# Optimization experiments

Measured on AMD Instinct MI355X. Metric: run time of the kernel, lower is better.

## Reference

```python
import jax, jax.numpy as jnp
import numpy as np

RATIO = 0.5
BN_EPS = 1e-5
L2_EPS = 1e-8


def setup_inputs() -> dict:
    key = jax.random.key(0)
    ks = jax.random.split(key, 8)
    B, L, D, E = 64, 577, 512, 1024
    H = E // 2  # MLP hidden = embed_dim // 2 = 512
    base_features = jax.random.normal(ks[0], (B, L, D), dtype=jnp.float32)
    atten = jax.random.uniform(ks[1], (B, L, L), dtype=jnp.float32)
    s_fc = 1.0 / np.sqrt(D)
    s_h = 1.0 / np.sqrt(H)
    return {
        "base_features": base_features,
        "atten": atten,
        "fc_w": jax.random.uniform(ks[2], (E, D), jnp.float32, -s_fc, s_fc),
        "fc_b": jax.random.uniform(ks[3], (E,), jnp.float32, -s_fc, s_fc),
        "mlp_w0": jax.random.uniform(ks[4], (H, D), jnp.float32, -s_fc, s_fc),
        "mlp_b0": jax.random.uniform(ks[5], (H,), jnp.float32, -s_fc, s_fc),
        "bn0_gamma": jnp.ones((H,), jnp.float32),
        "bn0_beta": jnp.zeros((H,), jnp.float32),
        "mlp_w1": jax.random.uniform(ks[6], (E, H), jnp.float32, -s_h, s_h),
        "mlp_b1": jax.random.uniform(ks[7], (E,), jnp.float32, -s_h, s_h),
    }


def _forward(base_features, atten, fc_w, fc_b, mlp_w0, mlp_b0,
             bn0_gamma, bn0_beta, mlp_w1, mlp_b1):
    B, L, D = base_features.shape
    k = int((L - 1) * RATIO)  # static: derived from shape

    # atten[:, :, 0] = -1; rank tokens by CLS-row attention atten[:, 0]
    scores = atten[:, 0].at[:, 0].set(-1.0)           # [B, L]
    idx = jax.lax.top_k(scores, k)[1]                 # [B, k]

    # gather selected tokens: [B, k, D]
    feats = jnp.take_along_axis(base_features, idx[:, :, None], axis=1)

    # l2norm over last dim (norm = sqrt(sum(x^2)) + eps, then divide)
    norm = jnp.sqrt(jnp.sum(feats * feats, axis=-1, keepdims=True)) + L2_EPS
    feats = feats / norm

    # MLP (num_layers=2): Linear -> BN(training-mode batch stats) -> ReLU -> Linear
    x = feats.reshape(B * k, D)
    h = x @ mlp_w0.T + mlp_b0                         # [B*k, H]
    mu = jnp.mean(h, axis=0)
    var = jnp.mean((h - mu) ** 2, axis=0)             # biased var, as torch BN
    h = jax.nn.relu(bn0_gamma * (h - mu) * jax.lax.rsqrt(var + BN_EPS) + bn0_beta)
    x_att = (h @ mlp_w1.T + mlp_b1).reshape(B, k, -1)  # [B, k, E]

    local = jnp.einsum('bkd,ed->bke', feats, fc_w) + fc_b + x_att

    # maxk_pool1d_var with k=1 and full lengths == max over sequence dim
    return jnp.max(local, axis=1).astype(jnp.float32)  # [B, E]


def reference(base_features, atten, fc_w, fc_b, mlp_w0, mlp_b0,
              bn0_gamma, bn0_beta, mlp_w1, mlp_b1):
    return _forward(base_features, atten, fc_w, fc_b, mlp_w0, mlp_b0,
                    bn0_gamma, bn0_beta, mlp_w1, mlp_b1)
```

## Files before the change

kernel.cpp:

```cpp
#include <hip/hip_runtime.h>
#include <math.h>

#define B_   64
#define L_   577
#define D_   512
#define E_   1024
#define H_   512
#define K_   288
#define N_   (B_ * K_)
#define KBIG 1024
#define MTILES (N_ / 128)

typedef __attribute__((ext_vector_type(8))) __bf16 bf16x8;
typedef __attribute__((ext_vector_type(4))) float f32x4;
typedef __attribute__((ext_vector_type(4))) unsigned short ushort4v;
typedef __attribute__((ext_vector_type(8))) unsigned short ushort8v;

#define OFF_WBIG    0
#define OFF_W0B     2097152
#define OFF_BIASBIG 2621440
#define OFF_SCSH    2625536
#define OFF_IDX     2629632
#define OFF_PSUM    2703360
#define OFF_PSQ     2998272
#define OFF_OUTENC  3293184
#define OFF_ABIG    3555328

static __device__ __forceinline__ unsigned short f2bf(float f) {
  unsigned int u = __builtin_bit_cast(unsigned int, f);
  u = (u + 0x7fffu + ((u >> 16) & 1u)) >> 16;
  return (unsigned short)u;
}
static __device__ __forceinline__ float bf2f(unsigned short s) {
  unsigned int u = ((unsigned int)s) << 16;
  return __builtin_bit_cast(float, u);
}

static __device__ __forceinline__ unsigned int encf(float f) {
  unsigned int u = __builtin_bit_cast(unsigned int, f);
  return (u & 0x80000000u) ? ~u : (u | 0x80000000u);
}
static __device__ __forceinline__ float decf(unsigned int e) {
  unsigned int u = (e & 0x80000000u) ? (e ^ 0x80000000u) : ~e;
  return __builtin_bit_cast(float, u);
}

#define GLOAD_LDS16(g, l)                                          \
  __builtin_amdgcn_global_load_lds(                                \
      (const __attribute__((address_space(1))) void*)(g),          \
      (__attribute__((address_space(3))) void*)(l), 16, 0, 0)

__global__ __launch_bounds__(256) void prep_kernel(
    const float* __restrict__ fc_w, const float* __restrict__ fc_b,
    const float* __restrict__ w0,   const float* __restrict__ w1,
    const float* __restrict__ b1,
    unsigned short* __restrict__ wbig, unsigned short* __restrict__ w0b,
    float* __restrict__ biasbig, unsigned int* __restrict__ outenc) {
  int gid = blockIdx.x * 256 + threadIdx.x;
  if (gid < 65536) outenc[gid] = 0u;
  if (gid < 262144) {
    int e  = gid >> 8;
    int c4 = gid & 255;
    float4 v;
    if (c4 < 128) v = ((const float4*)(fc_w + e * D_))[c4];
    else          v = ((const float4*)(w1   + e * H_))[c4 - 128];
    ushort4v o = { f2bf(v.x), f2bf(v.y), f2bf(v.z), f2bf(v.w) };
    ((ushort4v*)wbig)[gid] = o;
    if (gid < E_) biasbig[gid] = fc_b[gid] + b1[gid];
  } else {
    int idx = gid - 262144;
    float4 v = ((const float4*)w0)[idx];
    ushort4v o = { f2bf(v.x), f2bf(v.y), f2bf(v.z), f2bf(v.w) };
    ((ushort4v*)w0b)[idx] = o;
  }
}

__global__ __launch_bounds__(256) void topk_kernel(
    const float* __restrict__ atten, int* __restrict__ idx) {
  __shared__ float s[L_];
  int b = blockIdx.x;
  const float* row = atten + (size_t)b * L_ * L_;
  for (int i = threadIdx.x; i < L_; i += 256) s[i] = (i == 0) ? -1.0f : row[i];
  __syncthreads();
  for (int i = threadIdx.x; i < L_; i += 256) {
    float si = s[i];
    int rank = 0;
    for (int j = 0; j < L_; ++j) {
      float sj = s[j];
      rank += (sj > si) || (sj == si && j < i);
    }
    if (rank < K_) idx[b * K_ + rank] = i;
  }
}

__global__ __launch_bounds__(128) void gather_norm_kernel(
    const float* __restrict__ base, const int* __restrict__ idx,
    unsigned short* __restrict__ abig) {
  int r = blockIdx.x;
  int b = r / K_;
  int tok = idx[r];
  const float* src = base + ((size_t)b * L_ + tok) * D_;
  float4 v = ((const float4*)src)[threadIdx.x];
  float ss = v.x * v.x + v.y * v.y + v.z * v.z + v.w * v.w;
  #pragma unroll
  for (int o = 32; o > 0; o >>= 1) ss += __shfl_down(ss, o, 64);
  __shared__ float wsum[2];
  if ((threadIdx.x & 63) == 0) wsum[threadIdx.x >> 6] = ss;
  __syncthreads();
  float total = wsum[0] + wsum[1];
  float inv = 1.0f / (sqrtf(total) + 1e-8f);
  ushort4v o4 = { f2bf(v.x * inv), f2bf(v.y * inv), f2bf(v.z * inv), f2bf(v.w * inv) };
  ((ushort4v*)(abig + (size_t)r * KBIG))[threadIdx.x] = o4;
}

template <int MODE>
__global__ __launch_bounds__(256) void gemm_mfma_kernel(
    const unsigned short* __restrict__ A, int lda,
    const unsigned short* __restrict__ W, int ldw,
    const float* __restrict__ bias,
    unsigned short* __restrict__ Cbf, int ldc, int K,
    float* __restrict__ psum, float* __restrict__ psq,
    unsigned int* __restrict__ outenc) {
  __shared__ unsigned short As[128 * 64];
  __shared__ unsigned short Bs[128 * 64];
  __shared__ float s_sum[4][64];
  __shared__ float s_sq[4][64];
  const int tid  = threadIdx.x;
  const int wave = tid >> 6;
  const int lane = tid & 63;
  const int m0 = blockIdx.x * 128;
  const int n0 = blockIdx.y * 128;

  const int srow = wave * 8 + (lane >> 3);
  const int g8   = ((lane & 7) ^ ((lane >> 3) & 7)) * 8;
  const int ldst = (wave * 64 + lane) * 8;

  const int quad = lane >> 4;
  const int l15  = lane & 15;
  const int wm = (wave & 1) * 64;
  const int wn = (wave >> 1) * 64;
  const int slot0 = quad ^ (l15 & 7);

  f32x4 acc[4][4];
  #pragma unroll
  for (int i = 0; i < 4; ++i)
    #pragma unroll
    for (int j = 0; j < 4; ++j)
      acc[i][j] = (f32x4)(0.0f);

  for (int k0 = 0; k0 < K; k0 += 64) {
    #pragma unroll
    for (int q = 0; q < 4; ++q) {
      GLOAD_LDS16(A + (size_t)(m0 + q * 32 + srow) * lda + k0 + g8,
                  &As[q * 2048 + ldst]);
      GLOAD_LDS16(W + (size_t)(n0 + q * 32 + srow) * ldw + k0 + g8,
                  &Bs[q * 2048 + ldst]);
    }
    __syncthreads();
    #pragma unroll
    for (int kk = 0; kk < 2; ++kk) {
      const int slot = slot0 ^ (kk * 4);
      bf16x8 af[4], bfr[4];
      #pragma unroll
      for (int i = 0; i < 4; ++i)
        af[i] = *(const bf16x8*)&As[(wm + 16 * i + l15) * 64 + slot * 8];
      #pragma unroll
      for (int j = 0; j < 4; ++j)
        bfr[j] = *(const bf16x8*)&Bs[(wn + 16 * j + l15) * 64 + slot * 8];
      #pragma unroll
      for (int i = 0; i < 4; ++i)
        #pragma unroll
        for (int j = 0; j < 4; ++j)
          acc[i][j] = __builtin_amdgcn_mfma_f32_16x16x32_bf16(af[i], bfr[j], acc[i][j], 0, 0, 0);
    }
    __syncthreads();
  }

  if (MODE == 0) {
    #pragma unroll
    for (int j = 0; j < 4; ++j) {
      int col = n0 + wn + 16 * j + l15;
      float bb = bias[col];
      float sm = 0.f, sq = 0.f;
      #pragma unroll
      for (int i = 0; i < 4; ++i) {
        int row_base = m0 + wm + 16 * i + quad * 4;
        #pragma unroll
        for (int r = 0; r < 4; ++r) {
          float v = acc[i][j][r] + bb;
          Cbf[(size_t)(row_base + r) * ldc + col] = f2bf(v);
          sm += v; sq += v * v;
        }
      }
      sm += __shfl_xor(sm, 16, 64); sm += __shfl_xor(sm, 32, 64);
      sq += __shfl_xor(sq, 16, 64); sq += __shfl_xor(sq, 32, 64);
      if (quad == 0) { s_sum[wave][j * 16 + l15] = sm; s_sq[wave][j * 16 + l15] = sq; }
    }
    __syncthreads();
    if (tid < 128) {
      int half = tid >> 6;
      int c = tid & 63;
      float sm = s_sum[half * 2][c] + s_sum[half * 2 + 1][c];
      float sq = s_sq[half * 2][c] + s_sq[half * 2 + 1][c];
      int col = n0 + half * 64 + c;
      psum[blockIdx.x * H_ + col] = sm;
      psq [blockIdx.x * H_ + col] = sq;
    }
  } else {
    #pragma unroll
    for (int j = 0; j < 4; ++j) {
      int col = n0 + wn + 16 * j + l15;
      float bb = bias[col];
      float m[4];
      #pragma unroll
      for (int i = 0; i < 4; ++i) {
        float v = fmaxf(fmaxf(acc[i][j][0], acc[i][j][1]),
                        fmaxf(acc[i][j][2], acc[i][j][3]));
        m[i] = v + bb;
      }
      #pragma unroll
      for (int i = 0; i < 4; ++i) {
        m[i] = fmaxf(m[i], __shfl_xor(m[i], 16, 64));
        m[i] = fmaxf(m[i], __shfl_xor(m[i], 32, 64));
      }
      if (quad == 0) {
        int base = m0 + wm;
        int b0i = (base) / K_;
        float cur = m[0]; int cb = b0i;
        #pragma unroll
        for (int i = 1; i < 4; ++i) {
          int bi = (base + 16 * i) / K_;
          if (bi == cb) cur = fmaxf(cur, m[i]);
          else { atomicMax(&outenc[cb * E_ + col], encf(cur)); cur = m[i]; cb = bi; }
        }
        atomicMax(&outenc[cb * E_ + col], encf(cur));
      }
    }
  }
}

__global__ __launch_bounds__(256) void bn_stats2_kernel(
    const float* __restrict__ psum, const float* __restrict__ psq,
    const float* __restrict__ gamma, const float* __restrict__ beta,
    float* __restrict__ scsh) {
  __shared__ float ls[8][32], lq[8][32];
  int c32 = threadIdx.x & 31;
  int slice = threadIdx.x >> 5;
  int c = blockIdx.x * 32 + c32;
  float S = 0.f, Q = 0.f;
  for (int i = 0; i < 18; ++i) {
    int mx = slice * 18 + i;
    S += psum[mx * H_ + c];
    Q += psq [mx * H_ + c];
  }
  ls[slice][c32] = S; lq[slice][c32] = Q;
  __syncthreads();
  if (slice == 0) {
    float St = 0.f, Qt = 0.f;
    #pragma unroll
    for (int s = 0; s < 8; ++s) { St += ls[s][c32]; Qt += lq[s][c32]; }
    const float invN = 1.0f / (float)N_;
    float mu = St * invN;
    float var = Qt * invN - mu * mu;
    float sc = rsqrtf(var + 1e-5f) * gamma[c];
    scsh[c] = sc;
    scsh[512 + c] = beta[c] - mu * sc;
  }
}

__global__ __launch_bounds__(256) void bn_apply_kernel(
    unsigned short* __restrict__ abig, const float* __restrict__ scsh) {
  int gid = blockIdx.x * 256 + threadIdx.x;
  int r = gid >> 6;
  int c8 = gid & 63;
  int c = c8 * 8;
  ushort8v* p = (ushort8v*)(abig + (size_t)r * KBIG + H_) + c8;
  ushort8v v = *p;
  float4 sca = *(const float4*)&scsh[c];
  float4 scb = *(const float4*)&scsh[c + 4];
  float4 sha = *(const float4*)&scsh[512 + c];
  float4 shb = *(const float4*)&scsh[512 + c + 4];
  float sc[8] = {sca.x, sca.y, sca.z, sca.w, scb.x, scb.y, scb.z, scb.w};
  float sh[8] = {sha.x, sha.y, sha.z, sha.w, shb.x, shb.y, shb.z, shb.w};
  ushort8v o;
  #pragma unroll
  for (int j = 0; j < 8; ++j) {
    float x = bf2f(v[j]);
    o[j] = f2bf(fmaxf(x * sc[j] + sh[j], 0.0f));
  }
  *p = o;
}

__global__ __launch_bounds__(256) void decode_kernel(
    const unsigned int* __restrict__ outenc, float* __restrict__ out) {
  int gid = blockIdx.x * 256 + threadIdx.x;
  out[gid] = decf(outenc[gid]);
}

extern "C" void kernel_launch(void* const* d_in, const int* in_sizes, int n_in,
                              void* d_out, int out_size, void* d_ws, size_t ws_size,
                              hipStream_t stream) {
  const float* base  = (const float*)d_in[0];
  const float* atten = (const float*)d_in[1];
  const float* fc_w  = (const float*)d_in[2];
  const float* fc_b  = (const float*)d_in[3];
  const float* w0    = (const float*)d_in[4];
  const float* b0    = (const float*)d_in[5];
  const float* gamma = (const float*)d_in[6];
  const float* beta  = (const float*)d_in[7];
  const float* w1    = (const float*)d_in[8];
  const float* b1    = (const float*)d_in[9];
  float* out = (float*)d_out;

  char* ws = (char*)d_ws;
  unsigned short* wbig    = (unsigned short*)(ws + OFF_WBIG);
  unsigned short* w0b     = (unsigned short*)(ws + OFF_W0B);
  float*          biasbig = (float*)(ws + OFF_BIASBIG);
  float*          scsh    = (float*)(ws + OFF_SCSH);
  int*            idx     = (int*)  (ws + OFF_IDX);
  float*          psum    = (float*)(ws + OFF_PSUM);
  float*          psq     = (float*)(ws + OFF_PSQ);
  unsigned int*   outenc  = (unsigned int*)(ws + OFF_OUTENC);
  unsigned short* abig    = (unsigned short*)(ws + OFF_ABIG);

  prep_kernel<<<1280, 256, 0, stream>>>(fc_w, fc_b, w0, w1, b1, wbig, w0b,
                                        biasbig, outenc);
  topk_kernel<<<B_, 256, 0, stream>>>(atten, idx);
  gather_norm_kernel<<<N_, 128, 0, stream>>>(base, idx, abig);
  {
    dim3 grid(MTILES, H_ / 128);
    gemm_mfma_kernel<0><<<grid, 256, 0, stream>>>(abig, KBIG, w0b, D_, b0,
                                                  abig + H_, KBIG, D_,
                                                  psum, psq, nullptr);
  }
  bn_stats2_kernel<<<16, 256, 0, stream>>>(psum, psq, gamma, beta, scsh);
  bn_apply_kernel<<<(N_ * 64) / 256, 256, 0, stream>>>(abig, scsh);
  {
    dim3 grid(MTILES, E_ / 128);
    gemm_mfma_kernel<1><<<grid, 256, 0, stream>>>(abig, KBIG, wbig, KBIG, biasbig,
                                                  nullptr, 0, KBIG, nullptr, nullptr,
                                                  outenc);
  }
  decode_kernel<<<(B_ * E_) / 256, 256, 0, stream>>>(outenc, out);
}
```

Baseline: 294.4 us.

## Fuse BN-apply into second GEMM loads, merge prep/topk, drop decode

Folds the BatchNorm scale/shift and ReLU into the A-tile load of the second GEMM for the hidden half of K, replacing async LDS loads there with register loads plus conversion. The top-k blocks are merged into the weight-prep kernel as extra blocks, and the output max now uses a float CAS loop written straight to the output, which removes the decode kernel. This cuts three launches and one full read/write pass over the hidden activations. In exchange the fused path gives up async global-to-LDS loads for half the K loop, and CAS loops may contend.

```diff
diff --git a/kernel.cpp b/kernel.cpp
--- a/kernel.cpp
+++ b/kernel.cpp
@@ -23,7 +23,6 @@
 #define OFF_IDX     2629632
 #define OFF_PSUM    2703360
 #define OFF_PSQ     2998272
-#define OFF_OUTENC  3293184
 #define OFF_ABIG    3555328
 
 static __device__ __forceinline__ unsigned short f2bf(float f) {
@@ -36,13 +35,16 @@
   return __builtin_bit_cast(float, u);
 }
 
-static __device__ __forceinline__ unsigned int encf(float f) {
-  unsigned int u = __builtin_bit_cast(unsigned int, f);
-  return (u & 0x80000000u) ? ~u : (u | 0x80000000u);
-}
-static __device__ __forceinline__ float decf(unsigned int e) {
-  unsigned int u = (e & 0x80000000u) ? (e ^ 0x80000000u) : ~e;
-  return __builtin_bit_cast(float, u);
+static __device__ __forceinline__ void atomicMaxF(float* addr, float val) {
+  unsigned int* ua = (unsigned int*)addr;
+  unsigned int vu = __builtin_bit_cast(unsigned int, val);
+  unsigned int cur = __builtin_bit_cast(unsigned int, -INFINITY);
+  while (true) {
+    unsigned int prev = atomicCAS(ua, cur, vu);
+    if (prev == cur) break;
+    if (__builtin_bit_cast(float, prev) >= val) break;
+    cur = prev;
+  }
 }
 
 #define GLOAD_LDS16(g, l)                                          \
@@ -50,46 +52,46 @@
       (const __attribute__((address_space(1))) void*)(g),          \
       (__attribute__((address_space(3))) void*)(l), 16, 0, 0)
 
-__global__ __launch_bounds__(256) void prep_kernel(
+__global__ __launch_bounds__(256) void prep_topk_kernel(
     const float* __restrict__ fc_w, const float* __restrict__ fc_b,
     const float* __restrict__ w0,   const float* __restrict__ w1,
-    const float* __restrict__ b1,
+    const float* __restrict__ b1,   const float* __restrict__ atten,
     unsigned short* __restrict__ wbig, unsigned short* __restrict__ w0b,
-    float* __restrict__ biasbig, unsigned int* __restrict__ outenc) {
-  int gid = blockIdx.x * 256 + threadIdx.x;
-  if (gid < 65536) outenc[gid] = 0u;
-  if (gid < 262144) {
-    int e  = gid >> 8;
-    int c4 = gid & 255;
-    float4 v;
-    if (c4 < 128) v = ((const float4*)(fc_w + e * D_))[c4];
-    else          v = ((const float4*)(w1   + e * H_))[c4 - 128];
-    ushort4v o = { f2bf(v.x), f2bf(v.y), f2bf(v.z), f2bf(v.w) };
-    ((ushort4v*)wbig)[gid] = o;
-    if (gid < E_) biasbig[gid] = fc_b[gid] + b1[gid];
+    float* __restrict__ biasbig, float* __restrict__ out,
+    int* __restrict__ idx) {
+  __shared__ float s[L_];
+  if (blockIdx.x < 1280) {
+    int gid = blockIdx.x * 256 + threadIdx.x;
+    if (gid < 65536) out[gid] = -INFINITY;
+    if (gid < 262144) {
+      int e  = gid >> 8;
+      int c4 = gid & 255;
+      float4 v;
+      if (c4 < 128) v = ((const float4*)(fc_w + e * D_))[c4];
+      else          v = ((const float4*)(w1   + e * H_))[c4 - 128];
+      ushort4v o = { f2bf(v.x), f2bf(v.y), f2bf(v.z), f2bf(v.w) };
+      ((ushort4v*)wbig)[gid] = o;
+      if (gid < E_) biasbig[gid] = fc_b[gid] + b1[gid];
+    } else {
+      int i2 = gid - 262144;
+      float4 v = ((const float4*)w0)[i2];
+      ushort4v o = { f2bf(v.x), f2bf(v.y), f2bf(v.z), f2bf(v.w) };
+      ((ushort4v*)w0b)[i2] = o;
+    }
   } else {
-    int idx = gid - 262144;
-    float4 v = ((const float4*)w0)[idx];
-    ushort4v o = { f2bf(v.x), f2bf(v.y), f2bf(v.z), f2bf(v.w) };
-    ((ushort4v*)w0b)[idx] = o;
-  }
-}
-
-__global__ __launch_bounds__(256) void topk_kernel(
-    const float* __restrict__ atten, int* __restrict__ idx) {
-  __shared__ float s[L_];
-  int b = blockIdx.x;
-  const float* row = atten + (size_t)b * L_ * L_;
-  for (int i = threadIdx.x; i < L_; i += 256) s[i] = (i == 0) ? -1.0f : row[i];
-  __syncthreads();
-  for (int i = threadIdx.x; i < L_; i += 256) {
-    float si = s[i];
-    int rank = 0;
-    for (int j = 0; j < L_; ++j) {
-      float sj = s[j];
-      rank += (sj > si) || (sj == si && j < i);
-    }
-    if (rank < K_) idx[b * K_ + rank] = i;
+    int b = blockIdx.x - 1280;
+    const float* row = atten + (size_t)b * L_ * L_;
+    for (int i = threadIdx.x; i < L_; i += 256) s[i] = (i == 0) ? -1.0f : row[i];
+    __syncthreads();
+    for (int i = threadIdx.x; i < L_; i += 256) {
+      float si = s[i];
+      int rank = 0;
+      for (int j = 0; j < L_; ++j) {
+        float sj = s[j];
+        rank += (sj > si) || (sj == si && j < i);
+      }
+      if (rank < K_) idx[b * K_ + rank] = i;
+    }
   }
 }
 
@@ -120,7 +122,7 @@
     const float* __restrict__ bias,
     unsigned short* __restrict__ Cbf, int ldc, int K,
     float* __restrict__ psum, float* __restrict__ psq,
-    unsigned int* __restrict__ outenc) {
+    const float* __restrict__ scsh, float* __restrict__ outf) {
   __shared__ unsigned short As[128 * 64];
   __shared__ unsigned short Bs[128 * 64];
   __shared__ float s_sum[4][64];
@@ -149,12 +151,36 @@
       acc[i][j] = (f32x4)(0.0f);
 
   for (int k0 = 0; k0 < K; k0 += 64) {
-    #pragma unroll
-    for (int q = 0; q < 4; ++q) {
-      GLOAD_LDS16(A + (size_t)(m0 + q * 32 + srow) * lda + k0 + g8,
-                  &As[q * 2048 + ldst]);
-      GLOAD_LDS16(W + (size_t)(n0 + q * 32 + srow) * ldw + k0 + g8,
-                  &Bs[q * 2048 + ldst]);
+    if (MODE == 0 || k0 < H_) {
+      #pragma unroll
+      for (int q = 0; q < 4; ++q) {
+        GLOAD_LDS16(A + (size_t)(m0 + q * 32 + srow) * lda + k0 + g8,
+                    &As[q * 2048 + ldst]);
+        GLOAD_LDS16(W + (size_t)(n0 + q * 32 + srow) * ldw + k0 + g8,
+                    &Bs[q * 2048 + ldst]);
+      }
+    } else {
+      #pragma unroll
+      for (int q = 0; q < 4; ++q)
+        GLOAD_LDS16(W + (size_t)(n0 + q * 32 + srow) * ldw + k0 + g8,
+                    &Bs[q * 2048 + ldst]);
+      const int c0 = k0 - H_ + g8;
+      float4 sa = *(const float4*)&scsh[c0];
+      float4 sb = *(const float4*)&scsh[c0 + 4];
+      float4 ha = *(const float4*)&scsh[512 + c0];
+      float4 hb = *(const float4*)&scsh[512 + c0 + 4];
+      float sc[8] = {sa.x, sa.y, sa.z, sa.w, sb.x, sb.y, sb.z, sb.w};
+      float sh[8] = {ha.x, ha.y, ha.z, ha.w, hb.x, hb.y, hb.z, hb.w};
+      #pragma unroll
+      for (int q = 0; q < 4; ++q) {
+        ushort8v v = *(const ushort8v*)(A + (size_t)(m0 + q * 32 + srow) * lda
+                                        + k0 + g8);
+        ushort8v o;
+        #pragma unroll
+        for (int j = 0; j < 8; ++j)
+          o[j] = f2bf(fmaxf(bf2f(v[j]) * sc[j] + sh[j], 0.0f));
+        *(ushort8v*)&As[q * 2048 + ldst] = o;
+      }
     }
     __syncthreads();
     #pragma unroll
@@ -225,15 +251,15 @@
       }
       if (quad == 0) {
         int base = m0 + wm;
-        int b0i = (base) / K_;
-        float cur = m[0]; int cb = b0i;
+        int cb = base / K_;
+        float cur = m[0];
         #pragma unroll
         for (int i = 1; i < 4; ++i) {
           int bi = (base + 16 * i) / K_;
           if (bi == cb) cur = fmaxf(cur, m[i]);
-          else { atomicMax(&outenc[cb * E_ + col], encf(cur)); cur = m[i]; cb = bi; }
+          else { atomicMaxF(&outf[cb * E_ + col], cur); cur = m[i]; cb = bi; }
         }
-        atomicMax(&outenc[cb * E_ + col], encf(cur));
+        atomicMaxF(&outf[cb * E_ + col], cur);
       }
     }
   }
@@ -266,35 +292,6 @@
     scsh[c] = sc;
     scsh[512 + c] = beta[c] - mu * sc;
   }
-}
-
-__global__ __launch_bounds__(256) void bn_apply_kernel(
-    unsigned short* __restrict__ abig, const float* __restrict__ scsh) {
-  int gid = blockIdx.x * 256 + threadIdx.x;
-  int r = gid >> 6;
-  int c8 = gid & 63;
-  int c = c8 * 8;
-  ushort8v* p = (ushort8v*)(abig + (size_t)r * KBIG + H_) + c8;
-  ushort8v v = *p;
-  float4 sca = *(const float4*)&scsh[c];
-  float4 scb = *(const float4*)&scsh[c + 4];
-  float4 sha = *(const float4*)&scsh[512 + c];
-  float4 shb = *(const float4*)&scsh[512 + c + 4];
-  float sc[8] = {sca.x, sca.y, sca.z, sca.w, scb.x, scb.y, scb.z, scb.w};
-  float sh[8] = {sha.x, sha.y, sha.z, sha.w, shb.x, shb.y, shb.z, shb.w};
-  ushort8v o;
-  #pragma unroll
-  for (int j = 0; j < 8; ++j) {
-    float x = bf2f(v[j]);
-    o[j] = f2bf(fmaxf(x * sc[j] + sh[j], 0.0f));
-  }
-  *p = o;
-}
-
-__global__ __launch_bounds__(256) void decode_kernel(
-    const unsigned int* __restrict__ outenc, float* __restrict__ out) {
-  int gid = blockIdx.x * 256 + threadIdx.x;
-  out[gid] = decf(outenc[gid]);
 }
 
 extern "C" void kernel_launch(void* const* d_in, const int* in_sizes, int n_in,
@@ -320,26 +317,22 @@
   int*            idx     = (int*)  (ws + OFF_IDX);
   float*          psum    = (float*)(ws + OFF_PSUM);
   float*          psq     = (float*)(ws + OFF_PSQ);
-  unsigned int*   outenc  = (unsigned int*)(ws + OFF_OUTENC);
   unsigned short* abig    = (unsigned short*)(ws + OFF_ABIG);
 
-  prep_kernel<<<1280, 256, 0, stream>>>(fc_w, fc_b, w0, w1, b1, wbig, w0b,
-                                        biasbig, outenc);
-  topk_kernel<<<B_, 256, 0, stream>>>(atten, idx);
+  prep_topk_kernel<<<1344, 256, 0, stream>>>(fc_w, fc_b, w0, w1, b1, atten,
+                                             wbig, w0b, biasbig, out, idx);
   gather_norm_kernel<<<N_, 128, 0, stream>>>(base, idx, abig);
   {
     dim3 grid(MTILES, H_ / 128);
     gemm_mfma_kernel<0><<<grid, 256, 0, stream>>>(abig, KBIG, w0b, D_, b0,
                                                   abig + H_, KBIG, D_,
-                                                  psum, psq, nullptr);
+                                                  psum, psq, nullptr, nullptr);
   }
   bn_stats2_kernel<<<16, 256, 0, stream>>>(psum, psq, gamma, beta, scsh);
-  bn_apply_kernel<<<(N_ * 64) / 256, 256, 0, stream>>>(abig, scsh);
   {
     dim3 grid(MTILES, E_ / 128);
     gemm_mfma_kernel<1><<<grid, 256, 0, stream>>>(abig, KBIG, wbig, KBIG, biasbig,
                                                   nullptr, 0, KBIG, nullptr, nullptr,
-                                                  outenc);
-  }
-  decode_kernel<<<(B_ * E_) / 256, 256, 0, stream>>>(outenc, out);
-}
+                                                  scsh, out);
+  }
+}
```

After: 296.8 us. No clear change (+0.8%).

## Merge prep and topk kernels, atomic BN stats, wave-per-row gather

Applied to the files above, without the earlier changes.

Fuses the weight-prep and top-k kernels into a single launch, with the extra blocks handling per-batch top-k ranking. The BN partial sums are now accumulated with global atomicAdd straight from the first GEMM epilogue, which removes the per-tile partial buffers and shrinks the stats kernel to a trivial per-column finalize. The gather/l2norm kernel maps one wave per row and reduces with shuffles only, so it no longer needs a shared-memory barrier. In exchange, atomics add contention on 1024 floats and make the floating-point summation order nondeterministic.

```diff
diff --git a/kernel.cpp b/kernel.cpp
--- a/kernel.cpp
+++ b/kernel.cpp
@@ -22,7 +22,6 @@
 #define OFF_SCSH    2625536
 #define OFF_IDX     2629632
 #define OFF_PSUM    2703360
-#define OFF_PSQ     2998272
 #define OFF_OUTENC  3293184
 #define OFF_ABIG    3555328
 
@@ -50,67 +49,70 @@
       (const __attribute__((address_space(1))) void*)(g),          \
       (__attribute__((address_space(3))) void*)(l), 16, 0, 0)
 
-__global__ __launch_bounds__(256) void prep_kernel(
+__global__ __launch_bounds__(256) void prep_topk_kernel(
     const float* __restrict__ fc_w, const float* __restrict__ fc_b,
     const float* __restrict__ w0,   const float* __restrict__ w1,
-    const float* __restrict__ b1,
+    const float* __restrict__ b1,   const float* __restrict__ atten,
     unsigned short* __restrict__ wbig, unsigned short* __restrict__ w0b,
-    float* __restrict__ biasbig, unsigned int* __restrict__ outenc) {
-  int gid = blockIdx.x * 256 + threadIdx.x;
-  if (gid < 65536) outenc[gid] = 0u;
-  if (gid < 262144) {
-    int e  = gid >> 8;
-    int c4 = gid & 255;
-    float4 v;
-    if (c4 < 128) v = ((const float4*)(fc_w + e * D_))[c4];
-    else          v = ((const float4*)(w1   + e * H_))[c4 - 128];
-    ushort4v o = { f2bf(v.x), f2bf(v.y), f2bf(v.z), f2bf(v.w) };
-    ((ushort4v*)wbig)[gid] = o;
-    if (gid < E_) biasbig[gid] = fc_b[gid] + b1[gid];
+    float* __restrict__ biasbig, unsigned int* __restrict__ outenc,
+    float* __restrict__ psumq, int* __restrict__ idx) {
+  __shared__ float s[L_];
+  if (blockIdx.x < 1280) {
+    int gid = blockIdx.x * 256 + threadIdx.x;
+    if (gid < 65536) outenc[gid] = 0u;
+    if (gid < 1024) psumq[gid] = 0.0f;
+    if (gid < 262144) {
+      int e  = gid >> 8;
+      int c4 = gid & 255;
+      float4 v;
+      if (c4 < 128) v = ((const float4*)(fc_w + e * D_))[c4];
+      else          v = ((const float4*)(w1   + e * H_))[c4 - 128];
+      ushort4v o = { f2bf(v.x), f2bf(v.y), f2bf(v.z), f2bf(v.w) };
+      ((ushort4v*)wbig)[gid] = o;
+      if (gid < E_) biasbig[gid] = fc_b[gid] + b1[gid];
+    } else {
+      int i2 = gid - 262144;
+      float4 v = ((const float4*)w0)[i2];
+      ushort4v o = { f2bf(v.x), f2bf(v.y), f2bf(v.z), f2bf(v.w) };
+      ((ushort4v*)w0b)[i2] = o;
+    }
   } else {
-    int idx = gid - 262144;
-    float4 v = ((const float4*)w0)[idx];
-    ushort4v o = { f2bf(v.x), f2bf(v.y), f2bf(v.z), f2bf(v.w) };
-    ((ushort4v*)w0b)[idx] = o;
-  }
-}
-
-__global__ __launch_bounds__(256) void topk_kernel(
-    const float* __restrict__ atten, int* __restrict__ idx) {
-  __shared__ float s[L_];
-  int b = blockIdx.x;
-  const float* row = atten + (size_t)b * L_ * L_;
-  for (int i = threadIdx.x; i < L_; i += 256) s[i] = (i == 0) ? -1.0f : row[i];
-  __syncthreads();
-  for (int i = threadIdx.x; i < L_; i += 256) {
-    float si = s[i];
-    int rank = 0;
-    for (int j = 0; j < L_; ++j) {
-      float sj = s[j];
-      rank += (sj > si) || (sj == si && j < i);
-    }
-    if (rank < K_) idx[b * K_ + rank] = i;
-  }
-}
-
-__global__ __launch_bounds__(128) void gather_norm_kernel(
+    int b = blockIdx.x - 1280;
+    const float* row = atten + (size_t)b * L_ * L_;
+    for (int i = threadIdx.x; i < L_; i += 256) s[i] = (i == 0) ? -1.0f : row[i];
+    __syncthreads();
+    for (int i = threadIdx.x; i < L_; i += 256) {
+      float si = s[i];
+      int rank = 0;
+      for (int j = 0; j < L_; ++j) {
+        float sj = s[j];
+        rank += (sj > si) || (sj == si && j < i);
+      }
+      if (rank < K_) idx[b * K_ + rank] = i;
+    }
+  }
+}
+
+__global__ __launch_bounds__(256) void gather_norm_kernel(
     const float* __restrict__ base, const int* __restrict__ idx,
     unsigned short* __restrict__ abig) {
-  int r = blockIdx.x;
+  int r = blockIdx.x * 4 + (threadIdx.x >> 6);
+  int lane = threadIdx.x & 63;
   int b = r / K_;
   int tok = idx[r];
   const float* src = base + ((size_t)b * L_ + tok) * D_;
-  float4 v = ((const float4*)src)[threadIdx.x];
-  float ss = v.x * v.x + v.y * v.y + v.z * v.z + v.w * v.w;
+  float4 v0 = ((const float4*)src)[lane];
+  float4 v1 = ((const float4*)src)[lane + 64];
+  float ss = v0.x * v0.x + v0.y * v0.y + v0.z * v0.z + v0.w * v0.w
+           + v1.x * v1.x + v1.y * v1.y + v1.z * v1.z + v1.w * v1.w;
   #pragma unroll
-  for (int o = 32; o > 0; o >>= 1) ss += __shfl_down(ss, o, 64);
-  __shared__ float wsum[2];
-  if ((threadIdx.x & 63) == 0) wsum[threadIdx.x >> 6] = ss;
-  __syncthreads();
-  float total = wsum[0] + wsum[1];
-  float inv = 1.0f / (sqrtf(total) + 1e-8f);
-  ushort4v o4 = { f2bf(v.x * inv), f2bf(v.y * inv), f2bf(v.z * inv), f2bf(v.w * inv) };
-  ((ushort4v*)(abig + (size_t)r * KBIG))[threadIdx.x] = o4;
+  for (int o = 1; o < 64; o <<= 1) ss += __shfl_xor(ss, o, 64);
+  float inv = 1.0f / (sqrtf(ss) + 1e-8f);
+  ushort4v o0 = { f2bf(v0.x * inv), f2bf(v0.y * inv), f2bf(v0.z * inv), f2bf(v0.w * inv) };
+  ushort4v o1 = { f2bf(v1.x * inv), f2bf(v1.y * inv), f2bf(v1.z * inv), f2bf(v1.w * inv) };
+  ushort4v* dst = (ushort4v*)(abig + (size_t)r * KBIG);
+  dst[lane] = o0;
+  dst[lane + 64] = o1;
 }
 
 template <int MODE>
@@ -123,8 +125,6 @@
     unsigned int* __restrict__ outenc) {
   __shared__ unsigned short As[128 * 64];
   __shared__ unsigned short Bs[128 * 64];
-  __shared__ float s_sum[4][64];
-  __shared__ float s_sq[4][64];
   const int tid  = threadIdx.x;
   const int wave = tid >> 6;
   const int lane = tid & 63;
@@ -194,17 +194,10 @@
       }
       sm += __shfl_xor(sm, 16, 64); sm += __shfl_xor(sm, 32, 64);
       sq += __shfl_xor(sq, 16, 64); sq += __shfl_xor(sq, 32, 64);
-      if (quad == 0) { s_sum[wave][j * 16 + l15] = sm; s_sq[wave][j * 16 + l15] = sq; }
-    }
-    __syncthreads();
-    if (tid < 128) {
-      int half = tid >> 6;
-      int c = tid & 63;
-      float sm = s_sum[half * 2][c] + s_sum[half * 2 + 1][c];
-      float sq = s_sq[half * 2][c] + s_sq[half * 2 + 1][c];
-      int col = n0 + half * 64 + c;
-      psum[blockIdx.x * H_ + col] = sm;
-      psq [blockIdx.x * H_ + col] = sq;
+      if (quad == 0) {
+        atomicAdd(&psum[col], sm);
+        atomicAdd(&psq[col], sq);
+      }
     }
   } else {
     #pragma unroll
@@ -225,8 +218,8 @@
       }
       if (quad == 0) {
         int base = m0 + wm;
-        int b0i = (base) / K_;
-        float cur = m[0]; int cb = b0i;
+        int cb = base / K_;
+        float cur = m[0];
         #pragma unroll
         for (int i = 1; i < 4; ++i) {
           int bi = (base + 16 * i) / K_;
@@ -243,29 +236,14 @@
     const float* __restrict__ psum, const float* __restrict__ psq,
     const float* __restrict__ gamma, const float* __restrict__ beta,
     float* __restrict__ scsh) {
-  __shared__ float ls[8][32], lq[8][32];
-  int c32 = threadIdx.x & 31;
-  int slice = threadIdx.x >> 5;
-  int c = blockIdx.x * 32 + c32;
-  float S = 0.f, Q = 0.f;
-  for (int i = 0; i < 18; ++i) {
-    int mx = slice * 18 + i;
-    S += psum[mx * H_ + c];
-    Q += psq [mx * H_ + c];
-  }
-  ls[slice][c32] = S; lq[slice][c32] = Q;
-  __syncthreads();
-  if (slice == 0) {
-    float St = 0.f, Qt = 0.f;
-    #pragma unroll
-    for (int s = 0; s < 8; ++s) { St += ls[s][c32]; Qt += lq[s][c32]; }
-    const float invN = 1.0f / (float)N_;
-    float mu = St * invN;
-    float var = Qt * invN - mu * mu;
-    float sc = rsqrtf(var + 1e-5f) * gamma[c];
-    scsh[c] = sc;
-    scsh[512 + c] = beta[c] - mu * sc;
-  }
+  int c = blockIdx.x * 256 + threadIdx.x;
+  float S = psum[c], Q = psq[c];
+  const float invN = 1.0f / (float)N_;
+  float mu = S * invN;
+  float var = Q * invN - mu * mu;
+  float sc = rsqrtf(var + 1e-5f) * gamma[c];
+  scsh[c] = sc;
+  scsh[512 + c] = beta[c] - mu * sc;
 }
 
 __global__ __launch_bounds__(256) void bn_apply_kernel(
@@ -319,21 +297,21 @@
   float*          scsh    = (float*)(ws + OFF_SCSH);
   int*            idx     = (int*)  (ws + OFF_IDX);
   float*          psum    = (float*)(ws + OFF_PSUM);
-  float*          psq     = (float*)(ws + OFF_PSQ);
+  float*          psq     = psum + 512;
   unsigned int*   outenc  = (unsigned int*)(ws + OFF_OUTENC);
   unsigned short* abig    = (unsigned short*)(ws + OFF_ABIG);
 
-  prep_kernel<<<1280, 256, 0, stream>>>(fc_w, fc_b, w0, w1, b1, wbig, w0b,
-                                        biasbig, outenc);
-  topk_kernel<<<B_, 256, 0, stream>>>(atten, idx);
-  gather_norm_kernel<<<N_, 128, 0, stream>>>(base, idx, abig);
+  prep_topk_kernel<<<1344, 256, 0, stream>>>(fc_w, fc_b, w0, w1, b1, atten,
+                                             wbig, w0b, biasbig, outenc,
+                                             psum, idx);
+  gather_norm_kernel<<<N_ / 4, 256, 0, stream>>>(base, idx, abig);
   {
     dim3 grid(MTILES, H_ / 128);
     gemm_mfma_kernel<0><<<grid, 256, 0, stream>>>(abig, KBIG, w0b, D_, b0,
                                                   abig + H_, KBIG, D_,
                                                   psum, psq, nullptr);
   }
-  bn_stats2_kernel<<<16, 256, 0, stream>>>(psum, psq, gamma, beta, scsh);
+  bn_stats2_kernel<<<2, 256, 0, stream>>>(psum, psq, gamma, beta, scsh);
   bn_apply_kernel<<<(N_ * 64) / 256, 256, 0, stream>>>(abig, scsh);
   {
     dim3 grid(MTILES, E_ / 128);
```

Result: no change. 297.7 us (+1.1%).
